# Optimization experiments

Measured on AMD Instinct MI355X. Metric: run time of the kernel, lower is better.

Reference implementation:

```python
import jax, jax.numpy as jnp
import numpy as np

N, K, D = 65536, 1024, 512


def setup_inputs() -> dict:
    key = jax.random.key(0)
    k1, k2, k3 = jax.random.split(key, 3)
    x = jax.random.normal(k1, (N, D), dtype=jnp.float32)
    y = jax.random.randint(k2, (N,), 0, K)  # true/assigned cluster labels
    centers = jax.random.normal(k3, (K, D), dtype=jnp.float32)  # nn.Parameter
    return {"x": x, "y": y, "centers": centers}


def reference(x, y, centers):
    # caldis: squared euclidean distance from every point to every center.
    # original expand+sub+square+sum without materializing [N, K, D]).
    x2 = jnp.sum(x * x, axis=1, keepdims=True)          # [N, 1]
    c2 = jnp.sum(centers * centers, axis=1)              # [K]
    distance = x2 - 2.0 * (x @ centers.T) + c2           # [N, K]

    # predict: torch.sort(distance)[1][:, 0] == index of the smallest distance
    ynew = jnp.argmin(distance, axis=1)                  # [N]

    # calwei + calloss: one-hot(y) * distance summed == gather distance[i, y[i]]
    loss = jnp.sum(jnp.take_along_axis(distance, y[:, None], axis=1))

    return loss, ynew
```

## Files before the change

kernel.cpp:

```cpp
#include <hip/hip_runtime.h>

#define NPTS 65536
#define KC   1024
#define DD   512

using bf16x8 = __attribute__((ext_vector_type(8))) __bf16;
using f32x4  = __attribute__((ext_vector_type(4))) float;

__device__ __forceinline__ void gld_lds16(const void* g, void* lds_base) {
  __builtin_amdgcn_global_load_lds(
      (const __attribute__((address_space(1))) unsigned int*)(uintptr_t)g,
      (__attribute__((address_space(3))) unsigned int*)(unsigned int)(uintptr_t)lds_base,
      16, 0, 0);
}

__device__ __forceinline__ uint2 pack4(const float4& v) {
  uint2 r;
  r.x = (__float_as_uint(v.x) >> 16) | (__float_as_uint(v.y) & 0xffff0000u);
  r.y = (__float_as_uint(v.z) >> 16) | (__float_as_uint(v.w) & 0xffff0000u);
  return r;
}


__global__ __launch_bounds__(256) void prep_kernel(
    const float* __restrict__ x, const int* __restrict__ y,
    const float* __restrict__ centers, uint4* __restrict__ xb,
    uint4* __restrict__ cb, float* __restrict__ c2,
    float* __restrict__ partial) {
  const int w = threadIdx.x >> 6, l = threadIdx.x & 63;
  if (blockIdx.x >= 4096) {
    const int row = (blockIdx.x - 4096) * 4 + w;
    const float4* cf4 = (const float4*)centers;
    float4 a = cf4[row * 128 + 2 * l];
    float4 b = cf4[row * 128 + 2 * l + 1];
    uint2 pa = pack4(a), pb = pack4(b);
    cb[row * 64 + l] = make_uint4(pa.x, pa.y, pb.x, pb.y);
    float s = a.x * a.x + a.y * a.y + a.z * a.z + a.w * a.w +
              b.x * b.x + b.y * b.y + b.z * b.z + b.w * b.w;
#pragma unroll
    for (int off = 32; off; off >>= 1) s += __shfl_down(s, off, 64);
    if (l == 0) c2[row] = s;
    return;
  }
  const int rbase = blockIdx.x * 16 + w * 4;
  const float4* xr = (const float4*)(x + (size_t)rbase * DD);
  float4 a[4], b[4];
#pragma unroll
  for (int r = 0; r < 4; r++) {
    a[r] = xr[r * 128 + 2 * l];
    b[r] = xr[r * 128 + 2 * l + 1];
  }
  int yr[4];
#pragma unroll
  for (int r = 0; r < 4; r++) yr[r] = y[rbase + r];
  float4 ca[4], cb4[4];
#pragma unroll
  for (int r = 0; r < 4; r++) {
    const float4* cr = (const float4*)(centers + (size_t)yr[r] * DD);
    ca[r]  = cr[2 * l];
    cb4[r] = cr[2 * l + 1];
  }
#pragma unroll
  for (int r = 0; r < 4; r++) {
    uint2 pa = pack4(a[r]), pb = pack4(b[r]);
    xb[(size_t)(rbase + r) * 64 + l] = make_uint4(pa.x, pa.y, pb.x, pb.y);
  }
  float s = 0.f;
#pragma unroll
  for (int r = 0; r < 4; r++) {
    float d0 = a[r].x - ca[r].x, d1 = a[r].y - ca[r].y;
    float d2 = a[r].z - ca[r].z, d3 = a[r].w - ca[r].w;
    float d4 = b[r].x - cb4[r].x, d5 = b[r].y - cb4[r].y;
    float d6 = b[r].z - cb4[r].z, d7 = b[r].w - cb4[r].w;
    s += d0 * d0 + d1 * d1 + d2 * d2 + d3 * d3 +
         d4 * d4 + d5 * d5 + d6 * d6 + d7 * d7;
  }
#pragma unroll
  for (int off = 32; off; off >>= 1) s += __shfl_down(s, off, 64);
  __shared__ float ps[4];
  if (l == 0) ps[w] = s;
  __syncthreads();
  if (threadIdx.x == 0) partial[blockIdx.x] = ps[0] + ps[1] + ps[2] + ps[3];
}

__global__ __launch_bounds__(512, 2) void gemm_argmin(
    const uint4* __restrict__ xb, const uint4* __restrict__ cb,
    const float* __restrict__ c2, const float* __restrict__ partial,
    float* __restrict__ loss_out, float* __restrict__ ynew_out) {
  __shared__ uint4 As[4096];
  __shared__ uint4 Bs[4096];
  __shared__ float c2s[KC];
  __shared__ float ls[8];

  const int t = threadIdx.x;
  const int w = t >> 6, l = t & 63;
  const int wm = w >> 1, wn = w & 1;
  const int q4 = l >> 4, m16 = l & 15;
  const int row0 = blockIdx.x * 256;

  c2s[t] = c2[t];
  c2s[t + 512] = c2[t + 512];

  const int srow = l >> 2;
  const int schk = (l & 3) ^ ((l >> 3) & 3);
  const uint4* aB = xb + ((size_t)(row0 + w * 16 + srow) * 64 + schk);
  const uint4* bB = cb + ((size_t)(w * 16 + srow) * 64 + schk);

  const int xs = q4 ^ ((m16 >> 1) & 3);

#pragma unroll
  for (int p = 0; p < 3; p++) {
    const int sp = p * 1024;
    const int oa = p * 4;
    gld_lds16(aB + oa, &As[sp + w * 64]);
    gld_lds16(aB + 8192 + oa, &As[sp + w * 64 + 512]);
    gld_lds16(bB + oa, &Bs[sp + w * 64]);
    gld_lds16(bB + 8192 + oa, &Bs[sp + w * 64 + 512]);
  }

  f32x4 acc[4][8];
#pragma unroll
  for (int i = 0; i < 4; i++)
#pragma unroll
    for (int j = 0; j < 8; j++) acc[i][j] = (f32x4){0.f, 0.f, 0.f, 0.f};

  float best[16];
  int bi_[16];
#pragma unroll
  for (int i = 0; i < 16; i++) { best[i] = 3.4e38f; bi_[i] = 0; }

  asm volatile("s_waitcnt vmcnt(8)" ::: "memory");
  __builtin_amdgcn_s_barrier();

#pragma unroll 1
  for (int tt = 0; tt < 64; ++tt) {
    const int bse = (tt & 3) * 1024;
    bf16x8 af[4], bf0[4], bf1[4];
#pragma unroll
    for (int i = 0; i < 4; i++)
      af[i] = *(const bf16x8*)&As[bse + (wm * 64 + i * 16 + m16) * 4 + xs];
#pragma unroll
    for (int j = 0; j < 4; j++)
      bf0[j] = *(const bf16x8*)&Bs[bse + (wn * 128 + j * 16 + m16) * 4 + xs];
    if (tt < 61) {
      const int s2 = ((tt + 3) & 3) * 1024;
      const int oa = ((tt + 3) & 15) * 4;
      gld_lds16(aB + oa, &As[s2 + w * 64]);
      gld_lds16(aB + 8192 + oa, &As[s2 + w * 64 + 512]);
    }
    __builtin_amdgcn_s_setprio(1);
#pragma unroll
    for (int j = 0; j < 4; j++)
#pragma unroll
      for (int i = 0; i < 4; i++)
        acc[i][j] = __builtin_amdgcn_mfma_f32_16x16x32_bf16(af[i], bf0[j], acc[i][j], 0, 0, 0);
    __builtin_amdgcn_s_setprio(0);
#pragma unroll
    for (int j = 0; j < 4; j++)
      bf1[j] = *(const bf16x8*)&Bs[bse + (wn * 128 + (j + 4) * 16 + m16) * 4 + xs];
    if (tt < 61) {
      const int s2 = ((tt + 3) & 3) * 1024;
      const int ob = ((tt + 3) >> 4) * 16384 + ((tt + 3) & 15) * 4;
      gld_lds16(bB + ob, &Bs[s2 + w * 64]);
      gld_lds16(bB + ob + 8192, &Bs[s2 + w * 64 + 512]);
    }
    __builtin_amdgcn_s_setprio(1);
#pragma unroll
    for (int j = 0; j < 4; j++)
#pragma unroll
      for (int i = 0; i < 4; i++)
        acc[i][j + 4] = __builtin_amdgcn_mfma_f32_16x16x32_bf16(af[i], bf1[j], acc[i][j + 4], 0, 0, 0);
    __builtin_amdgcn_s_setprio(0);

    if ((tt & 15) == 15) {
      const int n0 = (tt >> 4) * 256;
#pragma unroll
      for (int j = 0; j < 8; j++) {
        const int n = n0 + wn * 128 + j * 16 + m16;
        const float cc = c2s[n];
#pragma unroll
        for (int i = 0; i < 4; i++)
#pragma unroll
          for (int r = 0; r < 4; r++) {
            float v = fmaf(-2.f, acc[i][j][r], cc);
            const int bi = i * 4 + r;
            if (v < best[bi]) { best[bi] = v; bi_[bi] = n; }
            acc[i][j][r] = 0.f;
          }
      }
    }

    if (tt < 61)       asm volatile("s_waitcnt vmcnt(8)" ::: "memory");
    else if (tt == 61) asm volatile("s_waitcnt vmcnt(4)" ::: "memory");
    else               asm volatile("s_waitcnt vmcnt(0)" ::: "memory");
    __builtin_amdgcn_s_barrier();
  }

  float* mv = (float*)As;
  int*   mi = (int*)((char*)As + 2048);
#pragma unroll
  for (int bi = 0; bi < 16; bi++) {
    float v = best[bi];
    int idx = bi_[bi];
#pragma unroll
    for (int off = 8; off; off >>= 1) {
      float ov = __shfl_xor(v, off, 64);
      int oi = __shfl_xor(idx, off, 64);
      if (ov < v || (ov == v && oi < idx)) { v = ov; idx = oi; }
    }
    if (m16 == 0) {
      const int m = wm * 64 + (bi >> 2) * 16 + q4 * 4 + (bi & 3);
      mv[wn * 256 + m] = v;
      mi[wn * 256 + m] = idx;
    }
  }
  __syncthreads();
  if (t < 256) {
    float v0 = mv[t], v1 = mv[256 + t];
    int i0 = mi[t], i1 = mi[256 + t];
    const int idx = (v1 < v0 || (v1 == v0 && i1 < i0)) ? i1 : i0;
    ynew_out[row0 + t] = (float)idx;
  }

  if (blockIdx.x == 0) {
    float s = 0.f;
#pragma unroll
    for (int j = 0; j < 8; j++) s += partial[t + 512 * j];
#pragma unroll
    for (int off = 32; off; off >>= 1) s += __shfl_down(s, off, 64);
    if (l == 0) ls[w] = s;
    __syncthreads();
    if (t == 0) {
      float tot = 0.f;
#pragma unroll
      for (int i = 0; i < 8; i++) tot += ls[i];
      loss_out[0] = tot;
    }
  }
}

__global__ __launch_bounds__(256) void loss_final(const float* __restrict__ partial,
                                                  float* __restrict__ out) {
  float s = 0.f;
#pragma unroll
  for (int j = 0; j < 64; j++) s += partial[threadIdx.x + 256 * j];
#pragma unroll
  for (int off = 32; off; off >>= 1) s += __shfl_down(s, off, 64);
  __shared__ float ps[4];
  if ((threadIdx.x & 63) == 0) ps[threadIdx.x >> 6] = s;
  __syncthreads();
  if (threadIdx.x == 0) out[0] = ps[0] + ps[1] + ps[2] + ps[3];
}


#define SLOT(row, oct) (16 * (oct) + (((row) & 15) ^ (((oct) & 2) << 1)))

__device__ __forceinline__ void split_pack(const float4& a, const float4& b,
                                           uint4& hi, uint4& lo) {
  float f[8] = {a.x, a.y, a.z, a.w, b.x, b.y, b.z, b.w};
  uint hw[4], lw[4];
#pragma unroll
  for (int i = 0; i < 4; i++) {
    uint e0 = __float_as_uint(f[2 * i]), e1 = __float_as_uint(f[2 * i + 1]);
    hw[i] = (e0 >> 16) | (e1 & 0xffff0000u);
    float l0 = f[2 * i]     - __uint_as_float(e0 & 0xffff0000u);
    float l1 = f[2 * i + 1] - __uint_as_float(e1 & 0xffff0000u);
    lw[i] = (__float_as_uint(l0) >> 16) | (__float_as_uint(l1) & 0xffff0000u);
  }
  hi = make_uint4(hw[0], hw[1], hw[2], hw[3]);
  lo = make_uint4(lw[0], lw[1], lw[2], lw[3]);
}

__global__ __launch_bounds__(256) void c2_kernel(const float* __restrict__ centers,
                                                 float* __restrict__ c2) {
  int wave = (blockIdx.x * 256 + threadIdx.x) >> 6;
  int lane = threadIdx.x & 63;
  const float4* c4 = (const float4*)(centers + (size_t)wave * DD);
  float s = 0.f;
#pragma unroll
  for (int j = 0; j < 2; j++) {
    float4 v = c4[lane + 64 * j];
    s += v.x * v.x + v.y * v.y + v.z * v.z + v.w * v.w;
  }
#pragma unroll
  for (int off = 32; off; off >>= 1) s += __shfl_down(s, off, 64);
  if (lane == 0) c2[wave] = s;
}

__global__ __launch_bounds__(256, 2) void argmin_fb(
    const float* __restrict__ x, const float* __restrict__ centers,
    const float* __restrict__ c2, float* __restrict__ ynew_out) {
  __shared__ uint4 Ah[512], Al[512], Bh[512], Bl[512];
  const int t = threadIdx.x;
  const int w = t >> 6, l = t & 63;
  const int wm = w >> 1, wn = w & 1;
  const size_t row0 = (size_t)blockIdx.x * 128;
  const int srow = t >> 1, h = t & 1;
  const int mt = srow >> 4;
  const int so0 = mt * 64 + SLOT(srow, 2 * h);
  const int so1 = mt * 64 + SLOT(srow, 2 * h + 1);
  const int rs = SLOT(l & 15, l >> 4);
  const float* xp = x + (row0 + srow) * DD + h * 16;
  float best[16];
  int bidx[16];
#pragma unroll
  for (int i = 0; i < 16; i++) { best[i] = 3.4e38f; bidx[i] = 0; }
  for (int n0 = 0; n0 < KC; n0 += 128) {
    const float* bp = centers + (size_t)(n0 + srow) * DD + h * 16;
    f32x4 acc[4][4];
#pragma unroll
    for (int i = 0; i < 4; i++)
#pragma unroll
      for (int j = 0; j < 4; j++) acc[i][j] = (f32x4){0.f, 0.f, 0.f, 0.f};
    float4 ra[4], rb[4];
#pragma unroll
    for (int q = 0; q < 4; q++) {
      ra[q] = *(const float4*)(xp + q * 4);
      rb[q] = *(const float4*)(bp + q * 4);
    }
    for (int ks = 0; ks < 16; ks++) {
      uint4 ah0, al0, ah1, al1, bh0, bl0, bh1, bl1;
      split_pack(ra[0], ra[1], ah0, al0);
      split_pack(ra[2], ra[3], ah1, al1);
      split_pack(rb[0], rb[1], bh0, bl0);
      split_pack(rb[2], rb[3], bh1, bl1);
      __syncthreads();
      Ah[so0] = ah0; Al[so0] = al0;
      Ah[so1] = ah1; Al[so1] = al1;
      Bh[so0] = bh0; Bl[so0] = bl0;
      Bh[so1] = bh1; Bl[so1] = bl1;
      __syncthreads();
      if (ks < 15) {
#pragma unroll
        for (int q = 0; q < 4; q++) {
          ra[q] = *(const float4*)(xp + (ks + 1) * 32 + q * 4);
          rb[q] = *(const float4*)(bp + (ks + 1) * 32 + q * 4);
        }
      }
      bf16x8 afh[4], afl[4], bfh[4], bfl[4];
#pragma unroll
      for (int i = 0; i < 4; i++) {
        afh[i] = *(const bf16x8*)&Ah[(wm * 4 + i) * 64 + rs];
        afl[i] = *(const bf16x8*)&Al[(wm * 4 + i) * 64 + rs];
        bfh[i] = *(const bf16x8*)&Bh[(wn * 4 + i) * 64 + rs];
        bfl[i] = *(const bf16x8*)&Bl[(wn * 4 + i) * 64 + rs];
      }
#pragma unroll
      for (int i = 0; i < 4; i++)
#pragma unroll
        for (int j = 0; j < 4; j++) {
          acc[i][j] = __builtin_amdgcn_mfma_f32_16x16x32_bf16(afh[i], bfh[j], acc[i][j], 0, 0, 0);
          acc[i][j] = __builtin_amdgcn_mfma_f32_16x16x32_bf16(afl[i], bfh[j], acc[i][j], 0, 0, 0);
          acc[i][j] = __builtin_amdgcn_mfma_f32_16x16x32_bf16(afh[i], bfl[j], acc[i][j], 0, 0, 0);
        }
    }
#pragma unroll
    for (int j = 0; j < 4; j++) {
      int n = n0 + wn * 64 + j * 16 + (l & 15);
      float cc = c2[n];
#pragma unroll
      for (int i = 0; i < 4; i++)
#pragma unroll
        for (int r = 0; r < 4; r++) {
          float v = fmaf(-2.f, acc[i][j][r], cc);
          int bi = i * 4 + r;
          if (v < best[bi]) { best[bi] = v; bidx[bi] = n; }
        }
    }
  }
#pragma unroll
  for (int bi = 0; bi < 16; bi++) {
    float v = best[bi];
    int idx = bidx[bi];
#pragma unroll
    for (int off = 8; off; off >>= 1) {
      float ov = __shfl_xor(v, off, 64);
      int oi = __shfl_xor(idx, off, 64);
      if (ov < v || (ov == v && oi < idx)) { v = ov; idx = oi; }
    }
    if ((l & 15) == 0) {
      int m = wm * 64 + (bi >> 2) * 16 + (l >> 4) * 4 + (bi & 3);
      ynew_out[row0 + m] = (float)idx;
    }
  }
}

__global__ __launch_bounds__(256) void loss_partial_fb(
    const float* __restrict__ x, const int* __restrict__ y,
    const float* __restrict__ centers, float* __restrict__ partial) {
  const int w = threadIdx.x >> 6, l = threadIdx.x & 63;
  const int row = blockIdx.x * 4 + w;
  const float4* x4 = (const float4*)(x + (size_t)row * DD);
  const float4* c4 = (const float4*)(centers + (size_t)y[row] * DD);
  float s = 0.f;
#pragma unroll
  for (int j = 0; j < 2; j++) {
    float4 xv = x4[2 * l + j], cv = c4[2 * l + j];
    float dx = xv.x - cv.x, dy = xv.y - cv.y, dz = xv.z - cv.z, dw = xv.w - cv.w;
    s += dx * dx + dy * dy + dz * dz + dw * dw;
  }
#pragma unroll
  for (int off = 32; off; off >>= 1) s += __shfl_down(s, off, 64);
  __shared__ float ps[4];
  if (l == 0) ps[w] = s;
  __syncthreads();
  if (threadIdx.x == 0) partial[blockIdx.x] = ps[0] + ps[1] + ps[2] + ps[3];
}


extern "C" void kernel_launch(void* const* d_in, const int* in_sizes, int n_in,
                              void* d_out, int out_size, void* d_ws, size_t ws_size,
                              hipStream_t stream) {
  const float* x       = (const float*)d_in[0];
  const int*   y       = (const int*)d_in[1];
  const float* centers = (const float*)d_in[2];
  float* out = (float*)d_out;

  const size_t xb_bytes = (size_t)NPTS * DD * 2;
  const size_t cb_bytes = (size_t)KC * DD * 2;
  const size_t need = xb_bytes + cb_bytes + (KC + NPTS / 4) * sizeof(float);

  if (ws_size >= need) {
    uint4* xb      = (uint4*)d_ws;
    uint4* cbp     = (uint4*)((char*)d_ws + xb_bytes);
    float* c2      = (float*)((char*)d_ws + xb_bytes + cb_bytes);
    float* partial = c2 + KC;
    prep_kernel<<<4096 + 256, 256, 0, stream>>>(x, y, centers, xb, cbp, c2, partial);
    gemm_argmin<<<NPTS / 256, 512, 0, stream>>>(xb, cbp, c2, partial, out, out + 1);
  } else {
    float* c2      = (float*)d_ws;
    float* partial = c2 + KC;
    c2_kernel<<<KC / 4, 256, 0, stream>>>(centers, c2);
    argmin_fb<<<NPTS / 128, 256, 0, stream>>>(x, centers, c2, out + 1);
    loss_partial_fb<<<NPTS / 4, 256, 0, stream>>>(x, y, centers, partial);
    loss_final<<<1, 256, 0, stream>>>(partial, out);
  }
}
```

Measured before the change: 277.1 us.

## Prefetch next tile's MFMA fragments into registers with ping-pong buffers

Restructures the main K loop so each tile's A fragments and first-half B fragments for the next tile are read from LDS into registers during the current tile's MFMA work. The loop is unrolled by two with ping-pong A fragment arrays. The vmcnt waits are tightened so the next stage has landed in LDS before the early reads. This hides LDS read latency behind MFMAs. In exchange it raises register pressure and leaves less global-load slack before each barrier.

```diff
diff --git a/kernel.cpp b/kernel.cpp
--- a/kernel.cpp
+++ b/kernel.cpp
@@ -105,7 +105,6 @@
   const int schk = (l & 3) ^ ((l >> 3) & 3);
   const uint4* aB = xb + ((size_t)(row0 + w * 16 + srow) * 64 + schk);
   const uint4* bB = cb + ((size_t)(w * 16 + srow) * 64 + schk);
-
   const int xs = q4 ^ ((m16 >> 1) & 3);
 
 #pragma unroll
@@ -129,72 +128,96 @@
 #pragma unroll
   for (int i = 0; i < 16; i++) { best[i] = 3.4e38f; bi_[i] = 0; }
 
-  asm volatile("s_waitcnt vmcnt(8)" ::: "memory");
+  asm volatile("s_waitcnt vmcnt(4)" ::: "memory");
   __builtin_amdgcn_s_barrier();
 
+  bf16x8 afA[4], afB[4], bfP[4], bfQ[4];
+#pragma unroll
+  for (int i = 0; i < 4; i++)
+    afA[i] = *(const bf16x8*)&As[(wm * 64 + i * 16 + m16) * 4 + xs];
+#pragma unroll
+  for (int j = 0; j < 4; j++)
+    bfP[j] = *(const bf16x8*)&Bs[(wn * 128 + j * 16 + m16) * 4 + xs];
+
+#define FOLD_P(P)                                                           \
+  {                                                                         \
+    const int n0f = (P) * 256;                                              \
+    _Pragma("unroll")                                                       \
+    for (int j = 0; j < 8; j++) {                                           \
+      const int n = n0f + wn * 128 + j * 16 + m16;                          \
+      const float cc = c2s[n];                                              \
+      _Pragma("unroll")                                                     \
+      for (int i = 0; i < 4; i++)                                           \
+        _Pragma("unroll")                                                   \
+        for (int r = 0; r < 4; r++) {                                       \
+          float v = fmaf(-2.f, acc[i][j][r], cc);                           \
+          const int bidx = i * 4 + r;                                       \
+          if (v < best[bidx]) { best[bidx] = v; bi_[bidx] = n; }            \
+          acc[i][j][r] = 0.f;                                               \
+        }                                                                   \
+    }                                                                       \
+  }
+
+#define TILE_BODY(T, AFC, AFN)                                              \
+  {                                                                         \
+    const int bse = ((T) & 3) * 1024;                                       \
+         \
+    if ((T) <= 60) {                                                        \
+      const int s2 = (((T) + 3) & 3) * 1024;                                \
+      const int oa = (((T) + 3) & 15) * 4;                                  \
+      gld_lds16(aB + oa, &As[s2 + w * 64]);                                 \
+      gld_lds16(aB + 8192 + oa, &As[s2 + w * 64 + 512]);                    \
+    }                                                                       \
+    if ((T) < 63) {                                                         \
+      const int bn = (((T) + 1) & 3) * 1024;                                \
+      _Pragma("unroll")                                                     \
+      for (int i = 0; i < 4; i++)                                           \
+        AFN[i] = *(const bf16x8*)&As[bn + (wm * 64 + i * 16 + m16) * 4 + xs]; \
+    }                                                                       \
+    _Pragma("unroll")                                                       \
+    for (int j = 0; j < 4; j++)                                             \
+      bfQ[j] = *(const bf16x8*)&Bs[bse + (wn * 128 + (j + 4) * 16 + m16) * 4 + xs]; \
+    __builtin_amdgcn_s_setprio(1);                                          \
+    _Pragma("unroll")                                                       \
+    for (int j = 0; j < 4; j++)                                             \
+      _Pragma("unroll")                                                     \
+      for (int i = 0; i < 4; i++)                                           \
+        acc[i][j] = __builtin_amdgcn_mfma_f32_16x16x32_bf16(AFC[i], bfP[j], acc[i][j], 0, 0, 0); \
+    __builtin_amdgcn_s_setprio(0);                                          \
+                 \
+    if ((T) <= 60) {                                                        \
+      const int s2 = (((T) + 3) & 3) * 1024;                                \
+      const int ob = (((T) + 3) >> 4) * 16384 + (((T) + 3) & 15) * 4;       \
+      gld_lds16(bB + ob, &Bs[s2 + w * 64]);                                 \
+      gld_lds16(bB + ob + 8192, &Bs[s2 + w * 64 + 512]);                    \
+    }                                                                       \
+    if ((T) < 63) {                                                         \
+      const int bn = (((T) + 1) & 3) * 1024;                                \
+      _Pragma("unroll")                                                     \
+      for (int j = 0; j < 4; j++)                                           \
+        bfP[j] = *(const bf16x8*)&Bs[bn + (wn * 128 + j * 16 + m16) * 4 + xs]; \
+    }                                                                       \
+    __builtin_amdgcn_s_setprio(1);                                          \
+    _Pragma("unroll")                                                       \
+    for (int j = 0; j < 4; j++)                                             \
+      _Pragma("unroll")                                                     \
+      for (int i = 0; i < 4; i++)                                           \
+        acc[i][j + 4] = __builtin_amdgcn_mfma_f32_16x16x32_bf16(AFC[i], bfQ[j], acc[i][j + 4], 0, 0, 0); \
+    __builtin_amdgcn_s_setprio(0);                                          \
+    if (((T) & 15) == 15) FOLD_P((T) >> 4);                                 \
+    if ((T) <= 60)      asm volatile("s_waitcnt vmcnt(4)" ::: "memory");    \
+    else if ((T) < 63)  asm volatile("s_waitcnt vmcnt(0)" ::: "memory");    \
+    __builtin_amdgcn_s_barrier();                                           \
+  }
+
 #pragma unroll 1
-  for (int tt = 0; tt < 64; ++tt) {
-    const int bse = (tt & 3) * 1024;
-    bf16x8 af[4], bf0[4], bf1[4];
-#pragma unroll
-    for (int i = 0; i < 4; i++)
-      af[i] = *(const bf16x8*)&As[bse + (wm * 64 + i * 16 + m16) * 4 + xs];
-#pragma unroll
-    for (int j = 0; j < 4; j++)
-      bf0[j] = *(const bf16x8*)&Bs[bse + (wn * 128 + j * 16 + m16) * 4 + xs];
-    if (tt < 61) {
-      const int s2 = ((tt + 3) & 3) * 1024;
-      const int oa = ((tt + 3) & 15) * 4;
-      gld_lds16(aB + oa, &As[s2 + w * 64]);
-      gld_lds16(aB + 8192 + oa, &As[s2 + w * 64 + 512]);
-    }
-    __builtin_amdgcn_s_setprio(1);
-#pragma unroll
-    for (int j = 0; j < 4; j++)
-#pragma unroll
-      for (int i = 0; i < 4; i++)
-        acc[i][j] = __builtin_amdgcn_mfma_f32_16x16x32_bf16(af[i], bf0[j], acc[i][j], 0, 0, 0);
-    __builtin_amdgcn_s_setprio(0);
-#pragma unroll
-    for (int j = 0; j < 4; j++)
-      bf1[j] = *(const bf16x8*)&Bs[bse + (wn * 128 + (j + 4) * 16 + m16) * 4 + xs];
-    if (tt < 61) {
-      const int s2 = ((tt + 3) & 3) * 1024;
-      const int ob = ((tt + 3) >> 4) * 16384 + ((tt + 3) & 15) * 4;
-      gld_lds16(bB + ob, &Bs[s2 + w * 64]);
-      gld_lds16(bB + ob + 8192, &Bs[s2 + w * 64 + 512]);
-    }
-    __builtin_amdgcn_s_setprio(1);
-#pragma unroll
-    for (int j = 0; j < 4; j++)
-#pragma unroll
-      for (int i = 0; i < 4; i++)
-        acc[i][j + 4] = __builtin_amdgcn_mfma_f32_16x16x32_bf16(af[i], bf1[j], acc[i][j + 4], 0, 0, 0);
-    __builtin_amdgcn_s_setprio(0);
-
-    if ((tt & 15) == 15) {
-      const int n0 = (tt >> 4) * 256;
-#pragma unroll
-      for (int j = 0; j < 8; j++) {
-        const int n = n0 + wn * 128 + j * 16 + m16;
-        const float cc = c2s[n];
-#pragma unroll
-        for (int i = 0; i < 4; i++)
-#pragma unroll
-          for (int r = 0; r < 4; r++) {
-            float v = fmaf(-2.f, acc[i][j][r], cc);
-            const int bi = i * 4 + r;
-            if (v < best[bi]) { best[bi] = v; bi_[bi] = n; }
-            acc[i][j][r] = 0.f;
-          }
-      }
-    }
-
-    if (tt < 61)       asm volatile("s_waitcnt vmcnt(8)" ::: "memory");
-    else if (tt == 61) asm volatile("s_waitcnt vmcnt(4)" ::: "memory");
-    else               asm volatile("s_waitcnt vmcnt(0)" ::: "memory");
-    __builtin_amdgcn_s_barrier();
-  }
+  for (int s = 0; s < 32; ++s) {
+    const int te = 2 * s;
+    TILE_BODY(te, afA, afB);
+    TILE_BODY(te + 1, afB, afA);
+  }
+#undef TILE_BODY
+#undef FOLD_P
 
   float* mv = (float*)As;
   int*   mi = (int*)((char*)As + 2048);
```

Measured after the change: 274.7 us. About the same (-0.9%).
